# Kernel optimization log

Measured on AMD Instinct MI355X. Metric: run time of the kernel, lower is better.

## Reference

```python
import math
import jax, jax.numpy as jnp
import numpy as np

D_MODEL = 4096
N_Q_HEADS = 32
N_KV_HEADS = 8
HEAD_DIM = D_MODEL // N_Q_HEADS  # 128
N_GROUPS = N_Q_HEADS // N_KV_HEADS  # 4
B, S = 1, 2048


def setup_inputs() -> dict:
    key = jax.random.key(0)
    k1, k2, k3, k4, k5 = jax.random.split(key, 5)
    scale = 1.0 / math.sqrt(D_MODEL)
    return {
        "x": jax.random.normal(k1, (B, S, D_MODEL), dtype=jnp.float32),
        "W_q": jax.random.normal(k2, (N_Q_HEADS * HEAD_DIM, D_MODEL), dtype=jnp.float32) * scale,
        "W_k": jax.random.normal(k3, (N_KV_HEADS * HEAD_DIM, D_MODEL), dtype=jnp.float32) * scale,
        "W_v": jax.random.normal(k4, (N_KV_HEADS * HEAD_DIM, D_MODEL), dtype=jnp.float32) * scale,
        "W_o": jax.random.normal(k5, (D_MODEL, D_MODEL), dtype=jnp.float32) * scale,
    }


def reference(x, W_q, W_k, W_v, W_o):
    Bsz, Sq, _ = x.shape
    # projections (nn.Linear, no bias): y = x @ W.T
    q = (x @ W_q.T).reshape(Bsz, Sq, N_Q_HEADS, HEAD_DIM).transpose(0, 2, 1, 3)   # [B,Hq,S,d]
    k = (x @ W_k.T).reshape(Bsz, Sq, N_KV_HEADS, HEAD_DIM).transpose(0, 2, 1, 3)  # [B,Hkv,S,d]
    v = (x @ W_v.T).reshape(Bsz, Sq, N_KV_HEADS, HEAD_DIM).transpose(0, 2, 1, 3)
    # physical KV head repeat (repeat_interleave over head dim)
    k_rep = jnp.repeat(k, N_GROUPS, axis=1)  # [B,Hq,S,d]
    v_rep = jnp.repeat(v, N_GROUPS, axis=1)
    scores = jnp.einsum("bhqd,bhkd->bhqk", q, k_rep) / math.sqrt(HEAD_DIM)
    attn = jax.nn.softmax(scores, axis=-1)  # no causal mask in the original
    out = jnp.einsum("bhqk,bhkd->bhqd", attn, v_rep)
    out = out.transpose(0, 2, 1, 3).reshape(Bsz, Sq, D_MODEL)
    out = out @ W_o.T
    # original returns first n_kv_heads slices of the REPEATED k/v as the "cache"
    return out, (k_rep[:, :N_KV_HEADS], v_rep[:, :N_KV_HEADS])
```

## Files before the change

kernel.cpp:

```cpp
#include <hip/hip_runtime.h>
#include <hip/hip_bf16.h>

typedef __bf16 bf16;
typedef float f32x4 __attribute__((ext_vector_type(4)));
typedef float f32x16 __attribute__((ext_vector_type(16)));
typedef bf16 bf16x8 __attribute__((ext_vector_type(8)));
typedef bf16 bf16x2 __attribute__((ext_vector_type(2)));
typedef unsigned u32x4 __attribute__((ext_vector_type(4)));

#define MFMA16(a,b,c) __builtin_amdgcn_mfma_f32_16x16x32_bf16((a),(b),(c),0,0,0)
#define MFMA32(a,b,c) __builtin_amdgcn_mfma_f32_32x32x16_bf16((a),(b),(c),0,0,0)

__device__ __forceinline__ void gload16(const void* g, void* l) {
    __builtin_amdgcn_global_load_lds((const __attribute__((address_space(1))) unsigned*)g,
                                     (__attribute__((address_space(3))) unsigned*)l, 16, 0, 0);
}

__device__ __forceinline__ unsigned pk(float lo, float hi) {
    bf16x2 t; t[0] = (bf16)lo; t[1] = (bf16)hi;
    return __builtin_bit_cast(unsigned, t);
}

__device__ __forceinline__ void cvt8(const float* __restrict__ in, bf16* __restrict__ out, int i) {
    const float4* p = (const float4*)in + (size_t)i * 2;
    float4 a = p[0], b = p[1];
    bf16x8 o;
    o[0]=(bf16)a.x; o[1]=(bf16)a.y; o[2]=(bf16)a.z; o[3]=(bf16)a.w;
    o[4]=(bf16)b.x; o[5]=(bf16)b.y; o[6]=(bf16)b.z; o[7]=(bf16)b.w;
    *((bf16x8*)out + i) = o;
}

__global__ __launch_bounds__(256) void cvt_all(const float* __restrict__ x, const float* __restrict__ wq,
                                               const float* __restrict__ wk, const float* __restrict__ wv,
                                               bf16* __restrict__ xb, bf16* __restrict__ wqkv) {
    int i = blockIdx.x * 256 + threadIdx.x;
    const float* src; bf16* dst; int n8;
    switch (blockIdx.y) {
        case 0: src = x;  dst = xb;                 n8 = 1048576; break;
        case 1: src = wq; dst = wqkv;               n8 = 2097152; break;
        case 2: src = wk; dst = wqkv + 16777216;    n8 = 524288;  break;
        default: src = wv; dst = wqkv + 20971520;   n8 = 524288;  break;
    }
    if (i < n8) cvt8(src, dst, i);
}

__global__ __launch_bounds__(256) void cvt_one(const float* __restrict__ in, bf16* __restrict__ out, int n8) {
    int i = blockIdx.x * 256 + threadIdx.x;
    if (i < n8) cvt8(in, out, i);
}

__device__ __forceinline__ void stage_tile(const bf16* __restrict__ A, const bf16* __restrict__ B,
                                           int K, int bm, int bn, int k0,
                                           bf16* As, bf16* Bs, int wv, int lane) {
#pragma unroll
    for (int i=0;i<4;++i) {
        int off = i*4096 + wv*1024 + lane*16;
        int row = off >> 7;
        int cg = (lane & 7) ^ (row & 7);
        gload16(A + (size_t)(bm+row)*K + k0 + cg*8, (char*)As + off);
    }
#pragma unroll
    for (int i=0;i<4;++i) {
        int off = i*4096 + wv*1024 + lane*16;
        int row = off >> 7;
        int cg = (lane & 7) ^ (row & 7);
        gload16(B + (size_t)(bn+row)*K + k0 + cg*8, (char*)Bs + off);
    }
}

__device__ __forceinline__ void gemm_core(const bf16* __restrict__ A, const bf16* __restrict__ B,
                                          int K, int bm, int bn, bf16* As, bf16* Bs, f32x4 (&acc)[4][4]) {
    const int tid = threadIdx.x, lane = tid & 63, wv = tid >> 6;
    const int wr = wv >> 1, wc = wv & 1, lr = lane & 15, ls = lane >> 4;

#pragma unroll
    for (int mm=0;mm<4;++mm)
#pragma unroll
        for (int nn=0;nn<4;++nn)
#pragma unroll
            for (int r=0;r<4;++r) acc[mm][nn][r] = 0.f;

    const int nt = K >> 6;
    stage_tile(A, B, K, bm, bn, 0,  As,        Bs,        wv, lane);
    stage_tile(A, B, K, bm, bn, 64, As + 8192, Bs + 8192, wv, lane);

    for (int t = 0; t < nt; ++t) {
        const int cur = t & 1;
        bf16* AsC = As + cur * 8192;
        bf16* BsC = Bs + cur * 8192;

        if (t < nt - 1) asm volatile("s_waitcnt vmcnt(8)" ::: "memory");
        else            asm volatile("s_waitcnt vmcnt(0)" ::: "memory");
        __builtin_amdgcn_s_barrier();
        __builtin_amdgcn_sched_barrier(0);

        bf16x8 af[2][4], bfr[2][4];
#pragma unroll
        for (int ks=0; ks<2; ++ks) {
#pragma unroll
            for (int mm=0;mm<4;++mm) {
                int row = wr*64 + mm*16 + lr;
                af[ks][mm] = *(const bf16x8*)((char*)AsC + row*128 + (((ks*4+ls) ^ (row&7))<<4));
            }
#pragma unroll
            for (int nn=0;nn<4;++nn) {
                int row = wc*64 + nn*16 + lr;
                bfr[ks][nn] = *(const bf16x8*)((char*)BsC + row*128 + (((ks*4+ls) ^ (row&7))<<4));
            }
        }
        asm volatile("s_waitcnt lgkmcnt(0)" ::: "memory");
        __builtin_amdgcn_sched_barrier(0);
        __builtin_amdgcn_s_barrier();
        __builtin_amdgcn_sched_barrier(0);

        if (t + 2 < nt)
            stage_tile(A, B, K, bm, bn, (t+2) << 6, AsC, BsC, wv, lane);

        __builtin_amdgcn_s_setprio(1);
#pragma unroll
        for (int ks=0; ks<2; ++ks)
#pragma unroll
            for (int mm=0;mm<4;++mm)
#pragma unroll
                for (int nn=0;nn<4;++nn)
                    acc[mm][nn] = MFMA16(af[ks][mm], bfr[ks][nn], acc[mm][nn]);
        __builtin_amdgcn_s_setprio(0);
    }
}

__global__ __launch_bounds__(256) void gemm_qkv(const bf16* __restrict__ A, const bf16* __restrict__ W,
                                                bf16* __restrict__ C, float qscale) {
    __shared__ __align__(16) bf16 As[2*128*64];
    __shared__ __align__(16) bf16 Bs[2*128*64];
    int flat = blockIdx.y * gridDim.x + blockIdx.x;
    int id = (flat & 7) * 96 + (flat >> 3);
    int bm = (id & 15) * 128, bn = (id >> 4) * 128;
    f32x4 acc[4][4];
    gemm_core(A, W, 4096, bm, bn, As, Bs, acc);

    const float s = (bn < 4096) ? qscale : 1.0f;
    const int lane = threadIdx.x & 63, wv = threadIdx.x >> 6;
    const int wr = wv >> 1, wc = wv & 1, lr = lane & 15, ls = lane >> 4;
#pragma unroll
    for (int mm=0;mm<4;++mm)
#pragma unroll
        for (int nn=0;nn<4;++nn)
#pragma unroll
            for (int r=0;r<4;++r) {
                int mg = bm + wr*64 + mm*16 + ls*4 + r;
                int ng = bn + wc*64 + nn*16 + lr;
                C[(size_t)mg * 6144 + ng] = (bf16)(acc[mm][nn][r] * s);
            }
}

__global__ __launch_bounds__(256) void gemm_o(const bf16* __restrict__ A, const bf16* __restrict__ B,
                                              float* __restrict__ Cp) {
    __shared__ __align__(16) bf16 As[2*128*64];
    __shared__ __align__(16) bf16 Bs[2*128*64];
    int flat = blockIdx.y * gridDim.x + blockIdx.x;
    int id = (flat & 7) * 64 + (flat >> 3);
    int bm = (id & 15) * 128, bn = (id >> 4) * 128;
    f32x4 acc[4][4];
    gemm_core(A, B, 4096, bm, bn, As, Bs, acc);

    const int lane = threadIdx.x & 63, wv = threadIdx.x >> 6;
    const int wr = wv >> 1, wc = wv & 1, lr = lane & 15, ls = lane >> 4;
#pragma unroll
    for (int mm=0;mm<4;++mm)
#pragma unroll
        for (int nn=0;nn<4;++nn)
#pragma unroll
            for (int r=0;r<4;++r) {
                int mg = bm + wr*64 + mm*16 + ls*4 + r;
                int ng = bn + wc*64 + nn*16 + lr;
                Cp[(size_t)mg * 4096 + ng] = acc[mm][nn][r];
            }
}

__global__ __launch_bounds__(256) void trans_cache(const bf16* __restrict__ QKVb, bf16* __restrict__ Vt,
                                                   float* __restrict__ cacheK, float* __restrict__ cacheV) {
    int b = blockIdx.x;
    if (b < 512) {
        __shared__ bf16 t[64][70];
        int dt = b & 15, st = b >> 4;
        int tt = threadIdx.x;
        int r = tt >> 2, c0 = (tt & 3) * 16;
#pragma unroll
        for (int i = 0; i < 2; ++i) {
            bf16x8 v = *(const bf16x8*)(QKVb + (size_t)(st*64 + r)*6144 + 5120 + dt*64 + c0 + i*8);
#pragma unroll
            for (int j = 0; j < 8; ++j) t[c0 + i*8 + j][r] = v[j];
        }
        __syncthreads();
        int c = tt >> 2, r0 = (tt & 3) * 16;
#pragma unroll
        for (int i = 0; i < 2; ++i) {
            bf16x8 v = *(const bf16x8*)(&t[c][r0 + i*8]);
            *(bf16x8*)(Vt + (size_t)(dt*64 + c)*2048 + st*64 + r0 + i*8) = v;
        }
    } else {
        int g = (b - 512) * 256 + threadIdx.x;
        int d8 = g & 15, s = (g >> 4) & 2047, j = (g >> 15) & 7, kv = g >> 18;
        int hk = j >> 2;
        bf16x8 v = *(const bf16x8*)(QKVb + (size_t)s*6144 + 4096 + kv*1024 + hk*128 + d8*8);
        float* dst = (kv ? cacheV : cacheK) + ((size_t)j*2048 + s)*128 + d8*8;
        float4 lo, hi;
        lo.x=(float)v[0]; lo.y=(float)v[1]; lo.z=(float)v[2]; lo.w=(float)v[3];
        hi.x=(float)v[4]; hi.y=(float)v[5]; hi.z=(float)v[6]; hi.w=(float)v[7];
        *(float4*)dst = lo;
        *(float4*)(dst + 4) = hi;
    }
}

__device__ __forceinline__ void stage_kv(const bf16* __restrict__ QKVb, const bf16* __restrict__ Vt,
                                         char* Ks, char* Vs, int kvh, int kt, int buf,
                                         int wv, int lane) {
#pragma unroll
    for (int i=0;i<2;++i) {
        int off = i*8192 + wv*1024 + lane*16;
        int row = off >> 8;
        int cg = (lane & 15) ^ (row & 7);
        gload16(QKVb + (size_t)(kt*64+row)*6144 + 4096 + kvh*128 + cg*8, Ks + buf*16384 + i*8192 + wv*1024);
    }
#pragma unroll
    for (int i=0;i<2;++i) {
        int off = i*8192 + wv*1024 + lane*16;
        int d = off >> 7;
        int cg = (lane & 7) ^ (d & 7);
        gload16(Vt + (size_t)(kvh*128+d)*2048 + kt*64 + cg*8, Vs + buf*16384 + i*8192 + wv*1024);
    }
}

__global__ __launch_bounds__(512) void flash_attn(const bf16* __restrict__ QKVb, const bf16* __restrict__ Vt,
                                                  bf16* __restrict__ AO) {
    __shared__ __align__(16) char Ks[2*16384];
    __shared__ __align__(16) char Vs[2*16384];
    const int tid = threadIdx.x, lane = tid & 63, wq = tid >> 6;
    const int l31 = lane & 31, hi = lane >> 5;
    const int h = blockIdx.y, kvh = h >> 2;
    const int q0w = blockIdx.x * 256 + wq * 32;

    bf16x8 qf[8];
#pragma unroll
    for (int f=0; f<8; ++f)
        qf[f] = *(const bf16x8*)(QKVb + (size_t)(q0w + l31)*6144 + h*128 + f*16 + hi*8);

    f32x16 acc[4];
#pragma unroll
    for (int db=0;db<4;++db)
#pragma unroll
        for (int r=0;r<16;++r) acc[db][r] = 0.f;
    float mrun = -1e30f, lrun = 0.f;

    stage_kv(QKVb, Vt, Ks, Vs, kvh, 0, 0, wq, lane);
    __syncthreads();

    for (int t = 0; t < 32; ++t) {
        const int cur = t & 1;
        if (t + 1 < 32) stage_kv(QKVb, Vt, Ks, Vs, kvh, t+1, cur^1, wq, lane);

        const char* KsB = Ks + cur*16384;
        f32x16 sc[2];
#pragma unroll
        for (int kc=0;kc<2;++kc)
#pragma unroll
            for (int r=0;r<16;++r) sc[kc][r] = 0.f;
#pragma unroll
        for (int f=0; f<8; ++f) {
            int r0 = l31, r1 = 32 + l31;
            bf16x8 k0 = *(const bf16x8*)(KsB + r0*256 + (((f*2+hi) ^ (r0&7))<<4));
            bf16x8 k1 = *(const bf16x8*)(KsB + r1*256 + (((f*2+hi) ^ (r1&7))<<4));
            sc[0] = MFMA32(k0, qf[f], sc[0]);
            sc[1] = MFMA32(k1, qf[f], sc[1]);
        }

        float tmax = sc[0][0];
#pragma unroll
        for (int r=1;r<16;++r) tmax = fmaxf(tmax, sc[0][r]);
#pragma unroll
        for (int r=0;r<16;++r) tmax = fmaxf(tmax, sc[1][r]);
        tmax = fmaxf(tmax, __shfl_xor(tmax, 32, 64));
        if (!__all(tmax <= mrun + 8.f)) {
            float mnew = fmaxf(mrun, tmax);
            float corr = __expf(mrun - mnew);
            mrun = mnew;
            lrun *= corr;
#pragma unroll
            for (int r=0;r<16;++r) {
                float cr = __shfl(corr, (r&3) + 8*(r>>2) + 4*hi, 64);
#pragma unroll
                for (int db=0;db<4;++db) acc[db][r] *= cr;
            }
        }
        float rs = 0.f;
#pragma unroll
        for (int kc=0;kc<2;++kc)
#pragma unroll
            for (int r=0;r<16;++r) { float e = __expf(sc[kc][r] - mrun); sc[kc][r] = e; rs += e; }
        rs += __shfl_xor(rs, 32, 64);
        lrun += rs;

        bf16x8 pa[4];
#pragma unroll
        for (int kb=0;kb<4;++kb) {
            const int kc = kb>>1, r0 = (kb&1)*8;
            unsigned a0 = pk(sc[kc][r0+0], sc[kc][r0+1]);
            unsigned a1 = pk(sc[kc][r0+2], sc[kc][r0+3]);
            unsigned b0 = pk(sc[kc][r0+4], sc[kc][r0+5]);
            unsigned b1 = pk(sc[kc][r0+6], sc[kc][r0+7]);
            unsigned sa0 = (unsigned)__shfl_xor((int)a0, 32, 64);
            unsigned sa1 = (unsigned)__shfl_xor((int)a1, 32, 64);
            unsigned sb0 = (unsigned)__shfl_xor((int)b0, 32, 64);
            unsigned sb1 = (unsigned)__shfl_xor((int)b1, 32, 64);
            u32x4 w;
            w[0] = hi ? sb0 : a0;
            w[1] = hi ? sb1 : a1;
            w[2] = hi ? b0 : sa0;
            w[3] = hi ? b1 : sa1;
            pa[kb] = __builtin_bit_cast(bf16x8, w);
        }

        const char* VsB = Vs + cur*16384;
#pragma unroll
        for (int db=0;db<4;++db) {
            const int d = db*32 + l31;
#pragma unroll
            for (int kb=0;kb<4;++kb) {
                bf16x8 vf = *(const bf16x8*)(VsB + d*128 + (((kb*2+hi) ^ (d&7))<<4));
                acc[db] = MFMA32(pa[kb], vf, acc[db]);
            }
        }
        __syncthreads();
    }

    float linv = 1.0f / lrun;
#pragma unroll
    for (int r=0;r<16;++r) {
        int crw = (r&3) + 8*(r>>2) + 4*hi;
        float lv = __shfl(linv, crw, 64);
        size_t qrow = (size_t)q0w + crw;
#pragma unroll
        for (int db=0;db<4;++db)
            AO[qrow*4096 + h*128 + db*32 + l31] = (bf16)(acc[db][r] * lv);
    }
}

extern "C" void kernel_launch(void* const* d_in, const int* in_sizes, int n_in,
                              void* d_out, int out_size, void* d_ws, size_t ws_size,
                              hipStream_t stream) {
    const float* x  = (const float*)d_in[0];
    const float* Wq = (const float*)d_in[1];
    const float* Wk = (const float*)d_in[2];
    const float* Wv = (const float*)d_in[3];
    const float* Wo = (const float*)d_in[4];

    bf16* xb   = (bf16*)d_ws;
    bf16* QKVb = xb + (size_t)8388608;
    bf16* Wqkv = QKVb + (size_t)12582912;
    bf16* Vt  = xb;
    bf16* Wob = Wqkv;
    bf16* AO  = Wqkv + (size_t)16777216;

    float* out = (float*)d_out;
    float* cacheK = out + (size_t)8388608;
    float* cacheV = cacheK + (size_t)2097152;

    const float qscale = 0.08838834764831845f;

    cvt_all<<<dim3(8192, 4), 256, 0, stream>>>(x, Wq, Wk, Wv, xb, Wqkv);
    gemm_qkv<<<dim3(16, 48), 256, 0, stream>>>(xb, Wqkv, QKVb, qscale);
    cvt_one<<<8192, 256, 0, stream>>>(Wo, Wob, 2097152);
    trans_cache<<<2560, 256, 0, stream>>>(QKVb, Vt, cacheK, cacheV);
    flash_attn<<<dim3(8, 32), 512, 0, stream>>>(QKVb, Vt, AO);
    gemm_o<<<dim3(16, 32), 256, 0, stream>>>(AO, Wob, out);
}
```

Measured before the change: 321.6 us.

## Use 256x256 tiles with 512-thread blocks for the QKV projection GEMM

Replaces the 128x128 QKV GEMM with a dedicated 256x256-tile kernel using 8 waves, each computing a 128x64 sub-tile, with double-buffered swizzled LDS staging. Larger tiles raise arithmetic intensity and halve global reloads of A and W per output. In exchange the grid drops from 768 to 192 blocks, fewer than the MI355X's 256 CUs so some sit idle, and each thread holds more accumulator registers, which risks lower occupancy.

```diff
diff --git a/kernel.cpp b/kernel.cpp
--- a/kernel.cpp
+++ b/kernel.cpp
@@ -49,6 +49,119 @@
     if (i < n8) cvt8(in, out, i);
 }
 
+__device__ __forceinline__ void stage_tile_256(const bf16* __restrict__ A, const bf16* __restrict__ B,
+                                               int K, int bm, int bn, int k0,
+                                               bf16* As, bf16* Bs, int tid) {
+#pragma unroll
+    for (int i=0;i<4;++i) {
+        int off = i*8192 + tid*16;
+        int row = off >> 7;
+        int cg  = (tid & 7) ^ (row & 7);
+        gload16(A + (size_t)(bm+row)*K + k0 + cg*8, (char*)As + off);
+    }
+#pragma unroll
+    for (int i=0;i<4;++i) {
+        int off = i*8192 + tid*16;
+        int row = off >> 7;
+        int cg  = (tid & 7) ^ (row & 7);
+        gload16(B + (size_t)(bn+row)*K + k0 + cg*8, (char*)Bs + off);
+    }
+}
+
+__global__ __launch_bounds__(512, 2) void gemm_qkv(const bf16* __restrict__ A, const bf16* __restrict__ W,
+                                                   bf16* __restrict__ C, float qscale) {
+    __shared__ __align__(16) bf16 As[2*256*64];
+    __shared__ __align__(16) bf16 Bs[2*256*64];
+    const int tid = threadIdx.x, lane = tid & 63, wv = tid >> 6;
+    const int wm = wv >> 2, wn = wv & 3;
+    const int lr = lane & 15, ls = lane >> 4;
+
+    int flat = blockIdx.y * 8 + blockIdx.x;
+    int id = (flat & 7) * 24 + (flat >> 3);
+    const int bm = (id & 7) * 256, bn = (id >> 3) * 256;
+    const int K = 4096, nt = 64;
+
+    f32x4 acc[8][4];
+#pragma unroll
+    for (int mm=0;mm<8;++mm)
+#pragma unroll
+        for (int nn=0;nn<4;++nn)
+#pragma unroll
+            for (int r=0;r<4;++r) acc[mm][nn][r] = 0.f;
+
+    stage_tile_256(A, W, K, bm, bn, 0,  As,         Bs,         tid);
+    stage_tile_256(A, W, K, bm, bn, 64, As + 16384, Bs + 16384, tid);
+
+    for (int t = 0; t < nt; ++t) {
+        const int cur = t & 1;
+        bf16* AsC = As + cur * 16384;
+        bf16* BsC = Bs + cur * 16384;
+
+        if (t < nt - 1) asm volatile("s_waitcnt vmcnt(8)" ::: "memory");
+        else            asm volatile("s_waitcnt vmcnt(0)" ::: "memory");
+        __builtin_amdgcn_s_barrier();
+        __builtin_amdgcn_sched_barrier(0);
+
+        bf16x8 af0[8], bf0[4];
+#pragma unroll
+        for (int mm=0;mm<8;++mm) {
+            int row = wm*128 + mm*16 + lr;
+            af0[mm] = *(const bf16x8*)((char*)AsC + row*128 + ((ls ^ (row&7))<<4));
+        }
+#pragma unroll
+        for (int nn=0;nn<4;++nn) {
+            int row = wn*64 + nn*16 + lr;
+            bf0[nn] = *(const bf16x8*)((char*)BsC + row*128 + ((ls ^ (row&7))<<4));
+        }
+        asm volatile("s_waitcnt lgkmcnt(0)" ::: "memory");
+        __builtin_amdgcn_sched_barrier(0);
+        __builtin_amdgcn_s_setprio(1);
+#pragma unroll
+        for (int mm=0;mm<8;++mm)
+#pragma unroll
+            for (int nn=0;nn<4;++nn) acc[mm][nn] = MFMA16(af0[mm], bf0[nn], acc[mm][nn]);
+        __builtin_amdgcn_s_setprio(0);
+
+        bf16x8 af1[8], bf1[4];
+#pragma unroll
+        for (int mm=0;mm<8;++mm) {
+            int row = wm*128 + mm*16 + lr;
+            af1[mm] = *(const bf16x8*)((char*)AsC + row*128 + (((4+ls) ^ (row&7))<<4));
+        }
+#pragma unroll
+        for (int nn=0;nn<4;++nn) {
+            int row = wn*64 + nn*16 + lr;
+            bf1[nn] = *(const bf16x8*)((char*)BsC + row*128 + (((4+ls) ^ (row&7))<<4));
+        }
+        asm volatile("s_waitcnt lgkmcnt(0)" ::: "memory");
+        __builtin_amdgcn_sched_barrier(0);
+        __builtin_amdgcn_s_barrier();
+        __builtin_amdgcn_sched_barrier(0);
+
+        if (t + 2 < nt)
+            stage_tile_256(A, W, K, bm, bn, (t+2) << 6, AsC, BsC, tid);
+
+        __builtin_amdgcn_s_setprio(1);
+#pragma unroll
+        for (int mm=0;mm<8;++mm)
+#pragma unroll
+            for (int nn=0;nn<4;++nn) acc[mm][nn] = MFMA16(af1[mm], bf1[nn], acc[mm][nn]);
+        __builtin_amdgcn_s_setprio(0);
+    }
+
+    const float s = (bn < 4096) ? qscale : 1.0f;
+#pragma unroll
+    for (int mm=0;mm<8;++mm)
+#pragma unroll
+        for (int nn=0;nn<4;++nn)
+#pragma unroll
+            for (int r=0;r<4;++r) {
+                int mg = bm + wm*128 + mm*16 + ls*4 + r;
+                int ng = bn + wn*64 + nn*16 + lr;
+                C[(size_t)mg * 6144 + ng] = (bf16)(acc[mm][nn][r] * s);
+            }
+}
+
 __device__ __forceinline__ void stage_tile(const bf16* __restrict__ A, const bf16* __restrict__ B,
                                            int K, int bm, int bn, int k0,
                                            bf16* As, bf16* Bs, int wv, int lane) {
@@ -126,31 +239,6 @@
                     acc[mm][nn] = MFMA16(af[ks][mm], bfr[ks][nn], acc[mm][nn]);
         __builtin_amdgcn_s_setprio(0);
     }
-}
-
-__global__ __launch_bounds__(256) void gemm_qkv(const bf16* __restrict__ A, const bf16* __restrict__ W,
-                                                bf16* __restrict__ C, float qscale) {
-    __shared__ __align__(16) bf16 As[2*128*64];
-    __shared__ __align__(16) bf16 Bs[2*128*64];
-    int flat = blockIdx.y * gridDim.x + blockIdx.x;
-    int id = (flat & 7) * 96 + (flat >> 3);
-    int bm = (id & 15) * 128, bn = (id >> 4) * 128;
-    f32x4 acc[4][4];
-    gemm_core(A, W, 4096, bm, bn, As, Bs, acc);
-
-    const float s = (bn < 4096) ? qscale : 1.0f;
-    const int lane = threadIdx.x & 63, wv = threadIdx.x >> 6;
-    const int wr = wv >> 1, wc = wv & 1, lr = lane & 15, ls = lane >> 4;
-#pragma unroll
-    for (int mm=0;mm<4;++mm)
-#pragma unroll
-        for (int nn=0;nn<4;++nn)
-#pragma unroll
-            for (int r=0;r<4;++r) {
-                int mg = bm + wr*64 + mm*16 + ls*4 + r;
-                int ng = bn + wc*64 + nn*16 + lr;
-                C[(size_t)mg * 6144 + ng] = (bf16)(acc[mm][nn][r] * s);
-            }
 }
 
 __global__ __launch_bounds__(256) void gemm_o(const bf16* __restrict__ A, const bf16* __restrict__ B,
@@ -368,7 +456,7 @@
     const float qscale = 0.08838834764831845f;
 
     cvt_all<<<dim3(8192, 4), 256, 0, stream>>>(x, Wq, Wk, Wv, xb, Wqkv);
-    gemm_qkv<<<dim3(16, 48), 256, 0, stream>>>(xb, Wqkv, QKVb, qscale);
+    gemm_qkv<<<dim3(8, 24), 512, 0, stream>>>(xb, Wqkv, QKVb, qscale);
     cvt_one<<<8192, 256, 0, stream>>>(Wo, Wob, 2097152);
     trans_cache<<<2560, 256, 0, stream>>>(QKVb, Vt, cacheK, cacheV);
     flash_attn<<<dim3(8, 32), 512, 0, stream>>>(QKVb, Vt, AO);
```

Result: faster. 314.8 us (-2.1%).
